# Optimization experiments

Hardware: AMD Instinct MI355X
Metric: run time of the kernel (lower is better)

The kernel has to match this reference:

```python
import jax, jax.numpy as jnp
import numpy as np

EPS = 0.1
P, C, T_MLP, C_MLP, B = 196, 768, 384, 3072, 64


def yat(x, W, b, alpha):
    # x: (..., in), W: (out, in), b: (out,), alpha: (1,)
    dot_nb = jnp.einsum('...i,oi->...o', x, W)          # no-bias dot (shared GEMM)
    dot = dot_nb + b
    w_norm_sq = jnp.sum(W * W, axis=1)                   # (out,)
    x_norm_sq = jnp.sum(x * x, axis=-1, keepdims=True)   # (..., 1)
    dist_sq = w_norm_sq + x_norm_sq - 2.0 * dot_nb
    out_f = W.shape[0]
    scale_base = out_f / np.log(out_f + 1.0)
    scale = jnp.sqrt(jnp.asarray(scale_base, x.dtype)) ** alpha[0]
    return scale * (dot * dot) / (dist_sq + EPS)


def setup_inputs() -> dict:
    key = jax.random.key(0)
    ks = jax.random.split(key, 7)
    x = jax.random.normal(ks[0], (B, P, C), dtype=jnp.float32)
    # token-mixing YAT: in=P, out=T_MLP
    tw = jax.random.normal(ks[1], (T_MLP, P), dtype=jnp.float32) / np.sqrt(P)
    tb = jnp.zeros((T_MLP,), jnp.float32)
    t_alpha = jnp.ones((1,), jnp.float32)
    # token-mixing linear: T_MLP -> P
    w2 = jax.random.uniform(ks[2], (P, T_MLP), jnp.float32, -1, 1) / np.sqrt(T_MLP)
    b2 = jax.random.uniform(ks[3], (P,), jnp.float32, -1, 1) / np.sqrt(T_MLP)
    # channel-mixing YAT: in=C, out=C_MLP
    cw = jax.random.normal(ks[4], (C_MLP, C), dtype=jnp.float32) / np.sqrt(C)
    cb = jnp.zeros((C_MLP,), jnp.float32)
    c_alpha = jnp.ones((1,), jnp.float32)
    # channel-mixing linear: C_MLP -> C
    w4 = jax.random.uniform(ks[5], (C, C_MLP), jnp.float32, -1, 1) / np.sqrt(C_MLP)
    b4 = jax.random.uniform(ks[6], (C,), jnp.float32, -1, 1) / np.sqrt(C_MLP)
    return {"x": x, "tw": tw, "tb": tb, "t_alpha": t_alpha, "w2": w2, "b2": b2,
            "cw": cw, "cb": cb, "c_alpha": c_alpha, "w4": w4, "b4": b4}


def reference(x, tw, tb, t_alpha, w2, b2, cw, cb, c_alpha, w4, b4):
    # Token mixing (operates over patch dim)
    shortcut = x
    xt = jnp.swapaxes(x, 1, 2)                 # (B, C, P)
    h = yat(xt, tw, tb, t_alpha)               # (B, C, T_MLP)
    h = jnp.einsum('bct,pt->bcp', h, w2) + b2  # (B, C, P)
    x = shortcut + jnp.swapaxes(h, 1, 2)
    # Channel mixing (operates over hidden dim)
    shortcut = x
    h = yat(x, cw, cb, c_alpha)                # (B, P, C_MLP)
    h = jnp.einsum('bpm,cm->bpc', h, w4) + b4  # (B, P, C)
    return shortcut + h
```

## Files before the change

kernel.cpp:

```cpp
#include <hip/hip_runtime.h>
#include <hip/hip_bf16.h>
#include <math.h>

#define B_   64
#define P_   196
#define PPAD 224
#define C_   768
#define TM_  384
#define CM_  3072
#define EPSY 0.1f

typedef unsigned short u16;
typedef __attribute__((ext_vector_type(8))) short bf16x8;
typedef __attribute__((ext_vector_type(4))) float f32x4;

__device__ __forceinline__ float bf2f(u16 v) {
    return __uint_as_float(((unsigned int)v) << 16);
}
__device__ __forceinline__ u16 f2bf(float f) {
    unsigned int u = __float_as_uint(f);
    unsigned int rounding = 0x7FFFu + ((u >> 16) & 1u);
    return (u16)((u + rounding) >> 16);
}

__device__ __forceinline__ void gl_lds16(const u16* g, u16* l) {
    __builtin_amdgcn_global_load_lds(
        (const __attribute__((address_space(1))) unsigned int*)g,
        (__attribute__((address_space(3))) unsigned int*)l,
        16, 0, 0);
}


__global__ __launch_bounds__(256) void k_prep_xT(const float* __restrict__ x,
                                                 u16* __restrict__ xT,
                                                 float* __restrict__ xn1) {
    __shared__ u16 tile[32][33];
    __shared__ float colsum[32];
    const int b = blockIdx.z, p0 = blockIdx.x * 32, c0 = blockIdx.y * 32;
    const int tx = threadIdx.x & 31, ty = threadIdx.x >> 5;
    if (threadIdx.x < 32) colsum[threadIdx.x] = 0.f;
    const float* xb = x + (size_t)b * P_ * C_;
    float s = 0.f;
    #pragma unroll
    for (int r = 0; r < 4; ++r) {
        int p = p0 + ty + r * 8;
        float v = (p < P_) ? xb[(size_t)p * C_ + c0 + tx] : 0.f;
        u16 h = f2bf(v);
        tile[ty + r * 8][tx] = h;
        float vb = bf2f(h);
        s = fmaf(vb, vb, s);
    }
    __syncthreads();
    u16* dst = xT + ((size_t)b * C_ + c0) * PPAD + p0;
    #pragma unroll
    for (int r = 0; r < 4; ++r) {
        int cl = ty + r * 8;
        dst[(size_t)cl * PPAD + tx] = tile[tx][cl];
    }
    atomicAdd(&colsum[tx], s);
    __syncthreads();
    if (threadIdx.x < 32)
        atomicAdd(&xn1[(size_t)b * C_ + c0 + threadIdx.x], colsum[threadIdx.x]);
}

__device__ __forceinline__ void pad_norm_body(const float* in, u16* outb, float* norm,
                                              int rows, int inlen, int outlen,
                                              int bid, int tid) {
    int wave = (bid * 256 + tid) >> 6;
    int lane = tid & 63;
    if (wave >= rows) return;
    const float* src = in + (size_t)wave * inlen;
    u16* dst = outb + (size_t)wave * outlen;
    float s = 0.f;
    for (int i = lane; i < outlen; i += 64) {
        float v = (i < inlen) ? src[i] : 0.f;
        u16 h = f2bf(v);
        dst[i] = h;
        float vv = bf2f(h);
        s = fmaf(vv, vv, s);
    }
    #pragma unroll
    for (int off = 32; off > 0; off >>= 1) s += __shfl_down(s, off, 64);
    if (lane == 0) norm[wave] = s;
}

__global__ __launch_bounds__(256) void k_prep_weights(
    const float* __restrict__ tw, u16* __restrict__ twb, float* __restrict__ twn,
    const float* __restrict__ cw, u16* __restrict__ cwb, float* __restrict__ cwn,
    const float* __restrict__ w2, u16* __restrict__ w2b,
    const float* __restrict__ w4, u16* __restrict__ w4b) {
    int bid = blockIdx.x, tid = threadIdx.x;
    if (bid < 96) {
        pad_norm_body(tw, twb, twn, TM_, P_, PPAD, bid, tid);
    } else if (bid < 864) {
        pad_norm_body(cw, cwb, cwn, CM_, C_, C_, bid - 96, tid);
    } else if (bid < 1248) {
        int idx = (bid - 864) * 256 + tid;
        int row = idx / TM_;
        w2b[idx] = (row < P_) ? f2bf(w2[(size_t)row * TM_ + (idx % TM_)]) : (u16)0;
    } else {
        int idx = (bid - 1248) * 256 + tid;
        float4 v = ((const float4*)w4)[idx];
        ushort4 o;
        o.x = f2bf(v.x); o.y = f2bf(v.y); o.z = f2bf(v.z); o.w = f2bf(v.w);
        ((ushort4*)w4b)[idx] = o;
    }
}

__device__ __forceinline__ void mfma_mainloop(
    const u16* __restrict__ A, const u16* __restrict__ B,
    int lda, int ldb, int kiters,
    f32x4 (&acc)[4][4], u16* As, u16* Bs) {
    const int t = threadIdx.x;
    const int w = t >> 6, l = t & 63;
    const int quad = l >> 4, l15 = l & 15;
    const int row0 = t >> 2, kc = (t & 3) * 8;

    const u16* pa0 = A + (size_t)row0 * lda + kc;
    const u16* pa1 = A + (size_t)(64 + row0) * lda + kc;
    const u16* pb0 = B + (size_t)row0 * ldb + kc;
    const u16* pb1 = B + (size_t)(64 + row0) * ldb + kc;

    u16* ldsA0 = As + w * 512;
    u16* ldsA1 = As + 2048 + w * 512;
    u16* ldsB0 = Bs + w * 512;
    u16* ldsB1 = Bs + 2048 + w * 512;

#define STAGE_(bsel, koff)                          \
    do {                                            \
        const int nb_ = (bsel) * 4096;              \
        gl_lds16(pa0 + (koff), ldsA0 + nb_);        \
        gl_lds16(pa1 + (koff), ldsA1 + nb_);        \
        gl_lds16(pb0 + (koff), ldsB0 + nb_);        \
        gl_lds16(pb1 + (koff), ldsB1 + nb_);        \
    } while (0)

    STAGE_(0, 0);
    if (kiters > 1) {
        STAGE_(1, 32);
        asm volatile("s_waitcnt vmcnt(4)" ::: "memory");
    } else {
        asm volatile("s_waitcnt vmcnt(0)" ::: "memory");
    }
    __builtin_amdgcn_s_barrier();

    int cur = 0;
    int koff = 64;
    for (int it = 0; it < kiters; ++it) {
        const u16* Aw = As + cur * 4096 + (w >> 1) * 2048;
        const u16* Bw = Bs + cur * 4096 + (w & 1) * 2048;
        bf16x8 af[4], bfr[4];
        #pragma unroll
        for (int i = 0; i < 4; ++i)
            af[i] = *(const bf16x8*)(Aw + ((i * 16 + l15) * 32 + quad * 8));
        #pragma unroll
        for (int j = 0; j < 4; ++j)
            bfr[j] = *(const bf16x8*)(Bw + ((j * 16 + l15) * 32 + quad * 8));
        asm volatile("s_waitcnt lgkmcnt(0)" ::: "memory");
        __builtin_amdgcn_sched_barrier(0);
        __builtin_amdgcn_s_barrier();
        const bool more2 = (it + 2 < kiters);
        if (more2) { STAGE_(cur, koff); koff += 32; }
        __builtin_amdgcn_s_setprio(1);
        #pragma unroll
        for (int i = 0; i < 4; ++i)
            #pragma unroll
            for (int j = 0; j < 4; ++j)
                acc[i][j] = __builtin_amdgcn_mfma_f32_16x16x32_bf16(af[i], bfr[j], acc[i][j], 0, 0, 0);
        __builtin_amdgcn_s_setprio(0);
        if (it + 1 < kiters) {
            if (more2) asm volatile("s_waitcnt vmcnt(4)" ::: "memory");
            else       asm volatile("s_waitcnt vmcnt(0)" ::: "memory");
            __builtin_amdgcn_s_barrier();
        }
        cur ^= 1;
    }
#undef STAGE_
}

#define MFMA_CORE(AP, BP, LDA, LDB, KITERS)                              \
    __shared__ u16 As[2 * 128 * 32];                                     \
    __shared__ u16 Bs[2 * 128 * 32];                                     \
    const int t = threadIdx.x;                                           \
    const int wid = t >> 6, lane = t & 63;                               \
    const int quad = lane >> 4, l15 = lane & 15;                         \
    f32x4 acc[4][4];                                                     \
    _Pragma("unroll")                                                    \
    for (int i = 0; i < 4; ++i)                                          \
        _Pragma("unroll")                                                \
        for (int j = 0; j < 4; ++j) acc[i][j] = (f32x4){0.f,0.f,0.f,0.f};\
    mfma_mainloop(AP, BP, LDA, LDB, KITERS, acc, As, Bs);                \
    const int rbase = m0 + (wid >> 1) * 64;                              \
    const int cbase = n0 + (wid & 1) * 64;

__device__ __forceinline__ void mfma256_mainloop(
    const u16* __restrict__ A, const u16* __restrict__ B,
    int lda, int ldb, int kiters,
    f32x4 (&acc)[8][4], u16* smem,
    int wr, int wc, int l15, int quad) {
    const int t = threadIdx.x;
    const int cxor = (quad * 8) ^ ((l15 & 3) * 8);

    const int off0 = t * 8;
    const int s0 = off0 ^ (((off0 >> 5) & 3) << 3);
    const int gr0 = s0 >> 5, gc0 = s0 & 31;
    const int off1 = 4096 + t * 8;
    const int s1 = off1 ^ (((off1 >> 5) & 3) << 3);
    const int gr1 = s1 >> 5, gc1 = s1 & 31;

    const u16* a0 = A + (size_t)gr0 * lda + gc0;
    const u16* a1 = A + (size_t)gr1 * lda + gc1;
    const u16* b0 = B + (size_t)gr0 * ldb + gc0;
    const u16* b1 = B + (size_t)gr1 * ldb + gc1;

#define STG256_(d, k0)                                   \
    do {                                                 \
        u16* sb_ = smem + (d) * 8192;                    \
        gl_lds16(a0 + (k0), sb_ + off0);                 \
        gl_lds16(a1 + (k0), sb_ + off1);                 \
        gl_lds16(b0 + (k0), sb_ + 16384 + off0);         \
        gl_lds16(b1 + (k0), sb_ + 16384 + off1);         \
    } while (0)

    STG256_(0, 0);
    if (kiters > 1) {
        STG256_(1, 32);
        asm volatile("s_waitcnt vmcnt(4)" ::: "memory");
    } else {
        asm volatile("s_waitcnt vmcnt(0)" ::: "memory");
    }
    __builtin_amdgcn_s_barrier();

    int cur = 0;
    for (int it = 0; it < kiters; ++it) {
        const u16* Ab = smem + cur * 8192;
        const u16* Bb = smem + 16384 + cur * 8192;
        bf16x8 bfr[4];
        #pragma unroll
        for (int n = 0; n < 4; ++n)
            bfr[n] = *(const bf16x8*)(Bb + (wc * 64 + n * 16 + l15) * 32 + cxor);
        __builtin_amdgcn_s_setprio(1);
        #pragma unroll
        for (int m = 0; m < 8; ++m) {
            bf16x8 af = *(const bf16x8*)(Ab + (wr * 128 + m * 16 + l15) * 32 + cxor);
            #pragma unroll
            for (int n = 0; n < 4; ++n)
                acc[m][n] = __builtin_amdgcn_mfma_f32_16x16x32_bf16(af, bfr[n], acc[m][n], 0, 0, 0);
        }
        __builtin_amdgcn_s_setprio(0);
        asm volatile("s_waitcnt lgkmcnt(0)" ::: "memory");
        __builtin_amdgcn_sched_barrier(0);
        __builtin_amdgcn_s_barrier();
        if (it + 2 < kiters) {
            STG256_(cur, (it + 2) * 32);
            asm volatile("s_waitcnt vmcnt(4)" ::: "memory");
            __builtin_amdgcn_s_barrier();
        } else if (it + 1 < kiters) {
            asm volatile("s_waitcnt vmcnt(0)" ::: "memory");
            __builtin_amdgcn_s_barrier();
        }
        cur ^= 1;
    }
#undef STG256_
}

__global__ __launch_bounds__(256) void k1_token_yat(
    const u16* __restrict__ xT, const u16* __restrict__ twb,
    const float* __restrict__ tb, const float* __restrict__ twn,
    const float* __restrict__ xn1, const float* __restrict__ alpha, float sb,
    u16* __restrict__ h1) {
    const int m0 = (blockIdx.x + blockIdx.y * 8) * 128;
    const int n0 = blockIdx.z * 128;
    MFMA_CORE(xT + (size_t)m0 * PPAD, twb + (size_t)n0 * PPAD, PPAD, PPAD, PPAD / 32)
    float scale = powf(sqrtf(sb), alpha[0]);
    #pragma unroll
    for (int i = 0; i < 4; ++i) {
        #pragma unroll
        for (int j = 0; j < 4; ++j) {
            int col = cbase + j * 16 + l15;
            float bn = tb[col], wnn = twn[col];
            #pragma unroll
            for (int reg = 0; reg < 4; ++reg) {
                int row = rbase + i * 16 + quad * 4 + reg;
                float dnb = acc[i][j][reg];
                float dot = dnb + bn;
                float dist = wnn + xn1[row] - 2.f * dnb;
                h1[(size_t)row * TM_ + col] = f2bf(scale * dot * dot / (dist + EPSY));
            }
        }
    }
}

__global__ __launch_bounds__(512) void k3_chan_yat(
    const u16* __restrict__ x1b, const u16* __restrict__ cwb,
    const float* __restrict__ cb, const float* __restrict__ cwn,
    const float* __restrict__ xn2, const float* __restrict__ alpha, float sb,
    u16* __restrict__ h3) {
    __shared__ __align__(16) u16 smem[32768];
    const int mt = blockIdx.x + blockIdx.y * 8;
    if (mt >= (B_ * P_) / 256) return;
    const int m0 = mt * 256;
    const int n0 = blockIdx.z * 256;
    const int t = threadIdx.x;
    const int wid = t >> 6, l = t & 63;
    const int wr = wid >> 2, wc = wid & 3;
    const int quad = l >> 4, l15 = l & 15;
    f32x4 acc[8][4];
    #pragma unroll
    for (int m = 0; m < 8; ++m)
        #pragma unroll
        for (int n = 0; n < 4; ++n) acc[m][n] = (f32x4){0.f, 0.f, 0.f, 0.f};
    mfma256_mainloop(x1b + (size_t)m0 * C_, cwb + (size_t)n0 * C_,
                     C_, C_, C_ / 32, acc, smem, wr, wc, l15, quad);
    const int rbase = m0 + wr * 128;
    const int cbase = n0 + wc * 64;
    float scale = powf(sqrtf(sb), alpha[0]);
    #pragma unroll
    for (int m = 0; m < 8; ++m) {
        #pragma unroll
        for (int n = 0; n < 4; ++n) {
            int col = cbase + n * 16 + l15;
            float bn = cb[col], wnn = cwn[col];
            #pragma unroll
            for (int reg = 0; reg < 4; ++reg) {
                int row = rbase + m * 16 + quad * 4 + reg;
                float dnb = acc[m][n][reg];
                float dot = dnb + bn;
                float dist = wnn + xn2[row] - 2.f * dnb;
                h3[(size_t)row * CM_ + col] = f2bf(scale * dot * dot / (dist + EPSY));
            }
        }
    }
}

__global__ __launch_bounds__(256) void k2_token_out(
    const u16* __restrict__ w2b, const u16* __restrict__ h1,
    const float* __restrict__ b2, const float* __restrict__ x,
    float* __restrict__ xn2, u16* __restrict__ x1b) {
    const int m0 = blockIdx.x * 128, n0 = blockIdx.y * 128;
    const u16* Bz = h1 + (size_t)blockIdx.z * C_ * TM_;
    MFMA_CORE(w2b + (size_t)m0 * TM_, Bz + (size_t)n0 * TM_, TM_, TM_, TM_ / 32)
    const float* rz = x + (size_t)blockIdx.z * P_ * C_;
    u16* oz = x1b + (size_t)blockIdx.z * P_ * C_;
    float* xrow = xn2 + (size_t)blockIdx.z * P_;
    #pragma unroll
    for (int i = 0; i < 4; ++i) {
        #pragma unroll
        for (int reg = 0; reg < 4; ++reg) {
            int row = rbase + i * 16 + quad * 4 + reg;
            if (row < P_) {
                float bm = b2[row];
                float s = 0.f;
                #pragma unroll
                for (int j = 0; j < 4; ++j) {
                    int col = cbase + j * 16 + l15;
                    float v = acc[i][j][reg] + bm + rz[(size_t)row * C_ + col];
                    u16 h = f2bf(v);
                    oz[(size_t)row * C_ + col] = h;
                    float vb = bf2f(h);
                    s = fmaf(vb, vb, s);
                }
                s += __shfl_xor(s, 1, 64);
                s += __shfl_xor(s, 2, 64);
                s += __shfl_xor(s, 4, 64);
                s += __shfl_xor(s, 8, 64);
                if (l15 == 0) atomicAdd(&xrow[row], s);
            }
        }
    }
}

__global__ __launch_bounds__(512) void k4_split(
    const u16* __restrict__ h3, const u16* __restrict__ w4b,
    u16* __restrict__ pbuf, int KK) {
    __shared__ __align__(16) u16 smem[32768];
    const int mt = blockIdx.x + blockIdx.y * 8;
    if (mt >= (B_ * P_) / 256) return;
    const int m0 = mt * 256;
    const int nz = blockIdx.z;
    const int n0 = (nz % 3) * 256;
    const int ks = nz / 3;
    const int kbase = ks * KK;
    const int t = threadIdx.x;
    const int wid = t >> 6, l = t & 63;
    const int wr = wid >> 2, wc = wid & 3;
    const int quad = l >> 4, l15 = l & 15;
    f32x4 acc[8][4];
    #pragma unroll
    for (int m = 0; m < 8; ++m)
        #pragma unroll
        for (int n = 0; n < 4; ++n) acc[m][n] = (f32x4){0.f, 0.f, 0.f, 0.f};
    mfma256_mainloop(h3 + (size_t)m0 * CM_ + kbase, w4b + (size_t)n0 * CM_ + kbase,
                     CM_, CM_, KK / 32, acc, smem, wr, wc, l15, quad);
    const int rbase = m0 + wr * 128;
    const int cbase = n0 + wc * 64;
    u16* dst = pbuf + (size_t)ks * ((size_t)B_ * P_ * C_);
    #pragma unroll
    for (int m = 0; m < 8; ++m) {
        #pragma unroll
        for (int n = 0; n < 4; ++n) {
            int col = cbase + n * 16 + l15;
            #pragma unroll
            for (int reg = 0; reg < 4; ++reg) {
                int row = rbase + m * 16 + quad * 4 + reg;
                dst[(size_t)row * C_ + col] = f2bf(acc[m][n][reg]);
            }
        }
    }
}

template <int NS>
__global__ __launch_bounds__(256) void k4_reduce(
    float* __restrict__ outp, const u16* __restrict__ pbuf,
    const u16* __restrict__ x1b, const float* __restrict__ b4) {
    int idx = blockIdx.x * 256 + threadIdx.x;
    int c = (idx * 4) % C_;
    ushort4 r = ((const ushort4*)x1b)[idx];
    float4 o;
    o.x = bf2f(r.x) + b4[c + 0];
    o.y = bf2f(r.y) + b4[c + 1];
    o.z = bf2f(r.z) + b4[c + 2];
    o.w = bf2f(r.w) + b4[c + 3];
    const size_t stride4 = (size_t)B_ * P_ * C_ / 4;
    #pragma unroll
    for (int s = 0; s < NS; ++s) {
        ushort4 p = ((const ushort4*)pbuf)[idx + s * stride4];
        o.x += bf2f(p.x); o.y += bf2f(p.y); o.z += bf2f(p.z); o.w += bf2f(p.w);
    }
    ((float4*)outp)[idx] = o;
}

__global__ __launch_bounds__(256) void gemm_k4_fb(
    const u16* __restrict__ A, const u16* __restrict__ Bmat,
    const float* __restrict__ biasN, const u16* __restrict__ resB,
    float* __restrict__ Fout) {
    __shared__ u16 As[128 * 32];
    __shared__ u16 Bs[64 * 32];
    const int t = threadIdx.x;
    const int wid = t >> 6, lane = t & 63;
    const int quad = lane >> 4, l15 = lane & 15;
    const int m0 = blockIdx.x * 128, n0 = blockIdx.y * 64;
    f32x4 acc[4][2];
    #pragma unroll
    for (int i = 0; i < 4; ++i)
        #pragma unroll
        for (int j = 0; j < 2; ++j) acc[i][j] = (f32x4){0.f, 0.f, 0.f, 0.f};
    const u16* Aw = As + (wid >> 1) * (64 * 32);
    const u16* Bw = Bs + (wid & 1) * (32 * 32);
    const int arow = t >> 2, akc = (t & 3) * 8;
    for (int k0 = 0; k0 < CM_; k0 += 32) {
        gl_lds16(A + (size_t)(m0 + arow) * CM_ + k0 + akc,      As + wid * 512);
        gl_lds16(A + (size_t)(m0 + 64 + arow) * CM_ + k0 + akc, As + 2048 + wid * 512);
        gl_lds16(Bmat + (size_t)(n0 + arow) * CM_ + k0 + akc,   Bs + wid * 512);
        __syncthreads();
        bf16x8 af[4], bfr[2];
        #pragma unroll
        for (int i = 0; i < 4; ++i)
            af[i] = *(const bf16x8*)(Aw + ((i * 16 + l15) * 32 + quad * 8));
        #pragma unroll
        for (int j = 0; j < 2; ++j)
            bfr[j] = *(const bf16x8*)(Bw + ((j * 16 + l15) * 32 + quad * 8));
        #pragma unroll
        for (int i = 0; i < 4; ++i)
            #pragma unroll
            for (int j = 0; j < 2; ++j)
                acc[i][j] = __builtin_amdgcn_mfma_f32_16x16x32_bf16(af[i], bfr[j], acc[i][j], 0, 0, 0);
        __syncthreads();
    }
    const int rbase = m0 + (wid >> 1) * 64;
    const int cbase = n0 + (wid & 1) * 32;
    #pragma unroll
    for (int i = 0; i < 4; ++i) {
        #pragma unroll
        for (int j = 0; j < 2; ++j) {
            int col = cbase + j * 16 + l15;
            float bn = biasN[col];
            #pragma unroll
            for (int reg = 0; reg < 4; ++reg) {
                int row = rbase + i * 16 + quad * 4 + reg;
                float v = acc[i][j][reg] + bn + bf2f(resB[(size_t)row * C_ + col]);
                Fout[(size_t)row * C_ + col] = v;
            }
        }
    }
}

extern "C" void kernel_launch(void* const* d_in, const int* in_sizes, int n_in,
                              void* d_out, int out_size, void* d_ws, size_t ws_size,
                              hipStream_t stream) {
    const float* x  = (const float*)d_in[0];
    const float* tw = (const float*)d_in[1];
    const float* tb = (const float*)d_in[2];
    const float* ta = (const float*)d_in[3];
    const float* w2 = (const float*)d_in[4];
    const float* b2 = (const float*)d_in[5];
    const float* cw = (const float*)d_in[6];
    const float* cb = (const float*)d_in[7];
    const float* ca = (const float*)d_in[8];
    const float* w4 = (const float*)d_in[9];
    const float* b4 = (const float*)d_in[10];
    float* out = (float*)d_out;

    char* ws = (char*)d_ws;
    u16* h1 = (u16*)ws;
    u16* xT = (u16*)(ws + 37748736);
    u16* h3 = (u16*)ws;
    size_t off = 77070336;
    u16* x1b = (u16*)(ws + off); off += (size_t)B_ * P_ * C_ * 2;
    u16* twb = (u16*)(ws + off); off += (size_t)TM_ * PPAD * 2;
    u16* w2b = (u16*)(ws + off); off += (size_t)256 * TM_ * 2;
    u16* cwb = (u16*)(ws + off); off += (size_t)CM_ * C_ * 2;
    u16* w4b = (u16*)(ws + off); off += (size_t)C_ * CM_ * 2;
    float* xn1 = (float*)(ws + off); off += (size_t)B_ * C_ * 4;
    float* xn2 = (float*)(ws + off); off += (size_t)B_ * P_ * 4;
    float* twn = (float*)(ws + off); off += (size_t)TM_ * 4;
    float* cwn = (float*)(ws + off); off += (size_t)CM_ * 4;
    u16* pbuf = (u16*)(ws + off);
    const size_t psz = (size_t)B_ * P_ * C_ * 2;

    int nsplit = 1;
    if (ws_size >= off + 4 * psz)      nsplit = 4;
    else if (ws_size >= off + 2 * psz) nsplit = 2;

    const float SBT = (float)TM_ / logf((float)TM_ + 1.0f);
    const float SBC = (float)CM_ / logf((float)CM_ + 1.0f);

    hipMemsetAsync(xn1, 0, (size_t)(B_ * C_ + B_ * P_) * 4, stream);
    k_prep_weights<<<3552, 256, 0, stream>>>(tw, twb, twn, cw, cwb, cwn,
                                             w2, w2b, w4, w4b);
    k_prep_xT<<<dim3(PPAD / 32, C_ / 32, B_), 256, 0, stream>>>(x, xT, xn1);

    k1_token_yat<<<dim3(8, 48, 3), 256, 0, stream>>>(
        xT, twb, tb, twn, xn1, ta, SBT, h1);

    k2_token_out<<<dim3(2, C_ / 128, B_), 256, 0, stream>>>(
        w2b, h1, b2, x, xn2, x1b);

    k3_chan_yat<<<dim3(8, 7, 12), 512, 0, stream>>>(
        x1b, cwb, cb, cwn, xn2, ca, SBC, h3);

    if (nsplit > 1) {
        k4_split<<<dim3(8, 7, 3 * nsplit), 512, 0, stream>>>(
            h3, w4b, pbuf, CM_ / nsplit);
        int n4 = B_ * P_ * C_ / 4;
        if (nsplit == 4)
            k4_reduce<4><<<(n4 + 255) / 256, 256, 0, stream>>>(out, pbuf, x1b, b4);
        else
            k4_reduce<2><<<(n4 + 255) / 256, 256, 0, stream>>>(out, pbuf, x1b, b4);
    } else {
        gemm_k4_fb<<<dim3(B_ * P_ / 128, C_ / 64), 256, 0, stream>>>(
            h3, w4b, b4, x1b, out);
    }
}
```

Baseline: 420.1 us.

## Replace 256x256 GEMM mainloop with 8-phase ping-pong schedule using K=64 tiles

Rewrites the shared mainloop of the two big channel-mixing GEMMs into an eight-phase schedule. Each K=64 tile is split into quadrant sub-MMAs, and per-half global-to-LDS loads are interleaved with barriers and priority toggles so loads overlap MFMA work. LDS per block doubles to 128KB and launch bounds request 2 waves per SIMD. The aim is to hide memory latency and cut per-iteration barrier overhead, at the cost of more LDS, more barriers and register pressure. It assumes the K tile count is even.

Result: faster. 366.2 us (-12.8%).

```diff
diff --git a/kernel.cpp b/kernel.cpp
--- a/kernel.cpp
+++ b/kernel.cpp
@@ -193,75 +193,122 @@
     const int rbase = m0 + (wid >> 1) * 64;                              \
     const int cbase = n0 + (wid & 1) * 64;
 
-__device__ __forceinline__ void mfma256_mainloop(
+#define PH_MID()  do { __builtin_amdgcn_sched_barrier(0);                 \
+    __builtin_amdgcn_s_barrier();                                         \
+    asm volatile("s_waitcnt lgkmcnt(0)" ::: "memory");                    \
+    __builtin_amdgcn_sched_barrier(0);                                    \
+    __builtin_amdgcn_s_setprio(1); } while (0)
+#define PH_END()  do { __builtin_amdgcn_s_setprio(0);                     \
+    __builtin_amdgcn_sched_barrier(0);                                    \
+    __builtin_amdgcn_s_barrier(); } while (0)
+#define PH_END_VM(n) do { __builtin_amdgcn_s_setprio(0);                  \
+    asm volatile("s_waitcnt vmcnt(" #n ")" ::: "memory");                 \
+    __builtin_amdgcn_sched_barrier(0);                                    \
+    __builtin_amdgcn_s_barrier(); } while (0)
+
+#define DSA(d, half, Ar)                                                  \
+    _Pragma("unroll")                                                     \
+    for (int mi = 0; mi < 4; ++mi) {                                      \
+        Ar[mi][0] = *(const bf16x8*)(aB0 + (d) * 16384 + ((half) * 4 + mi) * 1024); \
+        Ar[mi][1] = *(const bf16x8*)(aB1 + (d) * 16384 + ((half) * 4 + mi) * 1024); \
+    }
+#define DSB(d, half, Br)                                                  \
+    _Pragma("unroll")                                                     \
+    for (int ni = 0; ni < 2; ++ni) {                                      \
+        Br[ni][0] = *(const bf16x8*)(bB0 + (d) * 16384 + ((half) * 2 + ni) * 1024); \
+        Br[ni][1] = *(const bf16x8*)(bB1 + (d) * 16384 + ((half) * 2 + ni) * 1024); \
+    }
+#define MMQ(mh, nh, Ar, Br)                                               \
+    _Pragma("unroll")                                                     \
+    for (int kk = 0; kk < 2; ++kk)                                        \
+        _Pragma("unroll")                                                 \
+        for (int mi = 0; mi < 4; ++mi)                                    \
+            _Pragma("unroll")                                             \
+            for (int ni = 0; ni < 2; ++ni)                                \
+                acc[(mh) * 4 + mi][(nh) * 2 + ni] =                       \
+                    __builtin_amdgcn_mfma_f32_16x16x32_bf16(              \
+                        Ar[mi][kk], Br[ni][kk],                           \
+                        acc[(mh) * 4 + mi][(nh) * 2 + ni], 0, 0, 0);
+#define STG(isB, d, half, T)                                              \
+    do {                                                                  \
+        const u16* g_ = (isB) ? gB : gA;                                  \
+        const int ld_ = (isB) ? ldb : lda;                                \
+        u16* s_ = smem + ((isB) ? 32768 : 0) + (d) * 16384 + (half) * 4096 + sdst; \
+        gl_lds16(g_ + (size_t)((half) * 64) * ld_ + (T) * 64, s_);        \
+        gl_lds16(g_ + (size_t)((half) * 64 + 128) * ld_ + (T) * 64, s_ + 8192); \
+    } while (0)
+
+__device__ __forceinline__ void mfma8p_mainloop(
     const u16* __restrict__ A, const u16* __restrict__ B,
-    int lda, int ldb, int kiters,
-    f32x4 (&acc)[8][4], u16* smem,
-    int wr, int wc, int l15, int quad) {
+    int lda, int ldb, int ntiles,
+    f32x4 (&acc)[8][4], u16* smem) {
     const int t = threadIdx.x;
-    const int cxor = (quad * 8) ^ ((l15 & 3) * 8);
-
-    const int off0 = t * 8;
-    const int s0 = off0 ^ (((off0 >> 5) & 3) << 3);
-    const int gr0 = s0 >> 5, gc0 = s0 & 31;
-    const int off1 = 4096 + t * 8;
-    const int s1 = off1 ^ (((off1 >> 5) & 3) << 3);
-    const int gr1 = s1 >> 5, gc1 = s1 & 31;
-
-    const u16* a0 = A + (size_t)gr0 * lda + gc0;
-    const u16* a1 = A + (size_t)gr1 * lda + gc1;
-    const u16* b0 = B + (size_t)gr0 * ldb + gc0;
-    const u16* b1 = B + (size_t)gr1 * ldb + gc1;
-
-#define STG256_(d, k0)                                   \
-    do {                                                 \
-        u16* sb_ = smem + (d) * 8192;                    \
-        gl_lds16(a0 + (k0), sb_ + off0);                 \
-        gl_lds16(a1 + (k0), sb_ + off1);                 \
-        gl_lds16(b0 + (k0), sb_ + 16384 + off0);         \
-        gl_lds16(b1 + (k0), sb_ + 16384 + off1);         \
-    } while (0)
-
-    STG256_(0, 0);
-    if (kiters > 1) {
-        STG256_(1, 32);
-        asm volatile("s_waitcnt vmcnt(4)" ::: "memory");
-    } else {
-        asm volatile("s_waitcnt vmcnt(0)" ::: "memory");
-    }
+    const int w = t >> 6, lane = t & 63;
+    const int wr = w >> 2, wc = w & 3;
+    const int quad = lane >> 4, l15 = lane & 15;
+
+    const int srow = w * 8 + (lane >> 3);
+    const int cofs = ((lane & 7) ^ (lane >> 3)) * 8;
+    const int sdst = w * 512 + lane * 8;
+    const u16* gA = A + (size_t)srow * lda + cofs;
+    const u16* gB = B + (size_t)srow * ldb + cofs;
+
+    const int q = (quad * 8) ^ ((l15 & 7) << 3);
+    const u16* aB0 = smem + (wr * 128 + l15) * 64 + q;
+    const u16* aB1 = smem + (wr * 128 + l15) * 64 + (q ^ 32);
+    const u16* bB0 = smem + 32768 + (wc * 64 + l15) * 64 + q;
+    const u16* bB1 = smem + 32768 + (wc * 64 + l15) * 64 + (q ^ 32);
+
+    STG(0, 0, 0, 0); STG(0, 0, 1, 0); STG(1, 0, 0, 0); STG(1, 0, 1, 0);
+    STG(0, 1, 0, 1); STG(1, 1, 1, 1); STG(0, 1, 1, 1);
+    asm volatile("s_waitcnt vmcnt(6)" ::: "memory");
     __builtin_amdgcn_s_barrier();
 
-    int cur = 0;
-    for (int it = 0; it < kiters; ++it) {
-        const u16* Ab = smem + cur * 8192;
-        const u16* Bb = smem + 16384 + cur * 8192;
-        bf16x8 bfr[4];
-        #pragma unroll
-        for (int n = 0; n < 4; ++n)
-            bfr[n] = *(const bf16x8*)(Bb + (wc * 64 + n * 16 + l15) * 32 + cxor);
-        __builtin_amdgcn_s_setprio(1);
-        #pragma unroll
-        for (int m = 0; m < 8; ++m) {
-            bf16x8 af = *(const bf16x8*)(Ab + (wr * 128 + m * 16 + l15) * 32 + cxor);
-            #pragma unroll
-            for (int n = 0; n < 4; ++n)
-                acc[m][n] = __builtin_amdgcn_mfma_f32_16x16x32_bf16(af, bfr[n], acc[m][n], 0, 0, 0);
-        }
-        __builtin_amdgcn_s_setprio(0);
-        asm volatile("s_waitcnt lgkmcnt(0)" ::: "memory");
-        __builtin_amdgcn_sched_barrier(0);
-        __builtin_amdgcn_s_barrier();
-        if (it + 2 < kiters) {
-            STG256_(cur, (it + 2) * 32);
-            asm volatile("s_waitcnt vmcnt(4)" ::: "memory");
-            __builtin_amdgcn_s_barrier();
-        } else if (it + 1 < kiters) {
-            asm volatile("s_waitcnt vmcnt(0)" ::: "memory");
-            __builtin_amdgcn_s_barrier();
-        }
-        cur ^= 1;
-    }
-#undef STG256_
+    bf16x8 a[4][2], b[2][2], c[2][2];
+    const int NI = ntiles >> 1;
+    for (int i = 0; i < NI - 1; ++i) {
+        const int T1t = 2 * i + 1, N0 = 2 * i + 2, N1 = 2 * i + 3;
+        DSA(0, 0, a) DSB(0, 0, b)
+        STG(1, 1, 0, T1t);
+        PH_MID(); MMQ(0, 0, a, b) PH_END();
+        DSB(0, 1, c)
+        STG(0, 0, 0, N0);
+        PH_MID(); MMQ(0, 1, a, c) PH_END();
+        DSA(0, 1, a)
+        STG(1, 0, 1, N0);
+        PH_MID(); MMQ(1, 1, a, c) PH_END();
+        STG(0, 0, 1, N0);
+        PH_MID(); MMQ(1, 0, a, b) PH_END_VM(6);
+        DSA(1, 0, a) DSB(1, 0, b)
+        STG(1, 0, 0, N0);
+        PH_MID(); MMQ(0, 0, a, b) PH_END();
+        DSB(1, 1, c)
+        STG(0, 1, 0, N1);
+        PH_MID(); MMQ(0, 1, a, c) PH_END();
+        DSA(1, 1, a)
+        STG(1, 1, 1, N1);
+        PH_MID(); MMQ(1, 1, a, c) PH_END();
+        STG(0, 1, 1, N1);
+        PH_MID(); MMQ(1, 0, a, b) PH_END_VM(6);
+    }
+    {
+        const int T1t = 2 * NI - 1;
+        DSA(0, 0, a) DSB(0, 0, b)
+        STG(1, 1, 0, T1t);
+        PH_MID(); MMQ(0, 0, a, b) PH_END();
+        DSB(0, 1, c)
+        PH_MID(); MMQ(0, 1, a, c) PH_END();
+        DSA(0, 1, a)
+        PH_MID(); MMQ(1, 1, a, c) PH_END();
+        PH_MID(); MMQ(1, 0, a, b) PH_END_VM(0);
+        DSA(1, 0, a) DSB(1, 0, b)
+        PH_MID(); MMQ(0, 0, a, b) PH_END();
+        DSB(1, 1, c)
+        PH_MID(); MMQ(0, 1, a, c) PH_END();
+        DSA(1, 1, a)
+        PH_MID(); MMQ(1, 1, a, c) PH_END();
+        PH_MID(); MMQ(1, 0, a, b) PH_END();
+    }
 }
 
 __global__ __launch_bounds__(256) void k1_token_yat(
@@ -291,27 +338,27 @@
     }
 }
 
-__global__ __launch_bounds__(512) void k3_chan_yat(
+__global__ __launch_bounds__(512, 2) void k3_chan_yat(
     const u16* __restrict__ x1b, const u16* __restrict__ cwb,
     const float* __restrict__ cb, const float* __restrict__ cwn,
     const float* __restrict__ xn2, const float* __restrict__ alpha, float sb,
     u16* __restrict__ h3) {
-    __shared__ __align__(16) u16 smem[32768];
+    __shared__ __align__(16) u16 smem[65536];
     const int mt = blockIdx.x + blockIdx.y * 8;
     if (mt >= (B_ * P_) / 256) return;
     const int m0 = mt * 256;
     const int n0 = blockIdx.z * 256;
     const int t = threadIdx.x;
-    const int wid = t >> 6, l = t & 63;
-    const int wr = wid >> 2, wc = wid & 3;
+    const int w = t >> 6, l = t & 63;
+    const int wr = w >> 2, wc = w & 3;
     const int quad = l >> 4, l15 = l & 15;
     f32x4 acc[8][4];
     #pragma unroll
     for (int m = 0; m < 8; ++m)
         #pragma unroll
         for (int n = 0; n < 4; ++n) acc[m][n] = (f32x4){0.f, 0.f, 0.f, 0.f};
-    mfma256_mainloop(x1b + (size_t)m0 * C_, cwb + (size_t)n0 * C_,
-                     C_, C_, C_ / 32, acc, smem, wr, wc, l15, quad);
+    mfma8p_mainloop(x1b + (size_t)m0 * C_, cwb + (size_t)n0 * C_,
+                    C_, C_, C_ / 64, acc, smem);
     const int rbase = m0 + wr * 128;
     const int cbase = n0 + wc * 64;
     float scale = powf(sqrtf(sb), alpha[0]);
@@ -370,10 +417,10 @@
     }
 }
 
-__global__ __launch_bounds__(512) void k4_split(
+__global__ __launch_bounds__(512, 2) void k4_split(
     const u16* __restrict__ h3, const u16* __restrict__ w4b,
     u16* __restrict__ pbuf, int KK) {
-    __shared__ __align__(16) u16 smem[32768];
+    __shared__ __align__(16) u16 smem[65536];
     const int mt = blockIdx.x + blockIdx.y * 8;
     if (mt >= (B_ * P_) / 256) return;
     const int m0 = mt * 256;
@@ -382,16 +429,16 @@
     const int ks = nz / 3;
     const int kbase = ks * KK;
     const int t = threadIdx.x;
-    const int wid = t >> 6, l = t & 63;
-    const int wr = wid >> 2, wc = wid & 3;
+    const int w = t >> 6, l = t & 63;
+    const int wr = w >> 2, wc = w & 3;
     const int quad = l >> 4, l15 = l & 15;
     f32x4 acc[8][4];
     #pragma unroll
     for (int m = 0; m < 8; ++m)
         #pragma unroll
         for (int n = 0; n < 4; ++n) acc[m][n] = (f32x4){0.f, 0.f, 0.f, 0.f};
-    mfma256_mainloop(h3 + (size_t)m0 * CM_ + kbase, w4b + (size_t)n0 * CM_ + kbase,
-                     CM_, CM_, KK / 32, acc, smem, wr, wc, l15, quad);
+    mfma8p_mainloop(h3 + (size_t)m0 * CM_ + kbase, w4b + (size_t)n0 * CM_ + kbase,
+                    CM_, CM_, KK / 64, acc, smem);
     const int rbase = m0 + wr * 128;
     const int cbase = n0 + wc * 64;
     u16* dst = pbuf + (size_t)ks * ((size_t)B_ * P_ * C_);
```
